# Performance work log

Hardware: AMD Instinct MI355X
Metric: run time of the kernel (lower is better)

The kernel has to match this reference:

```python
import jax, jax.numpy as jnp
import numpy as np

N_NODES = 50000
N_EDGES = 1600000
IN_CH = 32
HID = 64
K = 2


def _dconv(X, edge_index, edge_weight, W, b):
    """Diffusion graph conv (torch_geometric_temporal DConv, K=2).

    X: [N, C_in], W: [2, K, C_in, C_out], b: [C_out].
    Direction 0: forward transition P_f = D_out^{-1} A  (applied as P_f^T X).
    Direction 1: backward transition P_b = D_in^{-1} A^T (applied as P_b^T X).
    """
    n = X.shape[0]
    row, col = edge_index[0], edge_index[1]
    deg_out = jax.ops.segment_sum(edge_weight, row, num_segments=n)  # out-degree (row sums of A)
    deg_in = jax.ops.segment_sum(edge_weight, col, num_segments=n)   # in-degree  (col sums of A)
    norm_out = edge_weight / deg_out[row]  # [E]
    norm_in = edge_weight / deg_in[col]    # [E]

    # k = 0 term: identity for both directions
    H = X @ (W[0, 0] + W[1, 0])

    # k = 1 term: one diffusion step in each direction
    # forward dir: out[i] = sum_{(j->i)} w/deg_out[j] * X[j]
    Tx_o = jax.ops.segment_sum(norm_out[:, None] * X[row], col, num_segments=n)
    # backward dir: out[i] = sum_{(i->j)} w/deg_in[j] * X[j]
    Tx_i = jax.ops.segment_sum(norm_in[:, None] * X[col], row, num_segments=n)
    H = H + Tx_o @ W[0, 1] + Tx_i @ W[1, 1]
    return H + b


def setup_inputs() -> dict:
    key = jax.random.key(0)
    ks = jax.random.split(key, 12)
    cat_ch = IN_CH + HID  # GRU concatenates [X, H]
    s = 1.0 / np.sqrt(cat_ch)
    inp = {
        "x": jax.random.normal(ks[0], (N_NODES, IN_CH), dtype=jnp.float32),
        "edge_index": jax.random.randint(ks[1], (2, N_EDGES), 0, N_NODES, dtype=jnp.int32),
        "edge_weight": jax.random.uniform(ks[2], (N_EDGES,), dtype=jnp.float32, minval=0.05, maxval=1.0),
        "Wz": jax.random.uniform(ks[3], (2, K, cat_ch, HID), dtype=jnp.float32, minval=-s, maxval=s),
        "bz": jnp.zeros((HID,), dtype=jnp.float32),
        "Wr": jax.random.uniform(ks[4], (2, K, cat_ch, HID), dtype=jnp.float32, minval=-s, maxval=s),
        "br": jnp.zeros((HID,), dtype=jnp.float32),
        "Wh": jax.random.uniform(ks[5], (2, K, cat_ch, HID), dtype=jnp.float32, minval=-s, maxval=s),
        "bh": jnp.zeros((HID,), dtype=jnp.float32),
        "Wlin": jax.random.uniform(ks[6], (HID, 1), dtype=jnp.float32, minval=-1.0 / np.sqrt(HID), maxval=1.0 / np.sqrt(HID)),
        "blin": jnp.zeros((1,), dtype=jnp.float32),
    }
    return inp


def reference(x, edge_index, edge_weight, Wz, bz, Wr, br, Wh, bh, Wlin, blin):
    n = x.shape[0]
    H0 = jnp.zeros((n, HID), dtype=x.dtype)  # initial hidden state (H=None)
    XH = jnp.concatenate([x, H0], axis=-1)   # [N, IN_CH+HID]
    Z = jax.nn.sigmoid(_dconv(XH, edge_index, edge_weight, Wz, bz))
    R = jax.nn.sigmoid(_dconv(XH, edge_index, edge_weight, Wr, br))
    XHR = jnp.concatenate([x, H0 * R], axis=-1)
    H_tilde = jnp.tanh(_dconv(XHR, edge_index, edge_weight, Wh, bh))
    H = Z * H0 + (1.0 - Z) * H_tilde
    out = jnp.maximum(H, 0.0) @ Wlin + blin  # ReLU then Linear(hidden, 1)
    return out
```

## Files before the change

### kernel.cpp

```cpp
#include <hip/hip_runtime.h>
#include <math.h>

#define N_NODES 50000
#define N_EDGES 1600000
#define IN_CH 32
#define HID 64

#define NBIN 782
#define BIN_SHIFT 6
#define CHUNK 8192
#define NCHK ((N_EDGES + CHUNK - 1) / CHUNK)
#define CNTG_N (2 * NBIN * NCHK)
#define CNTG_N4 (CNTG_N / 4)
#define SCAN_BLOCKS ((CNTG_N4 + 1023) / 1024)
#define FG_CAP 2560

#define PREP_WPREP_BLOCKS 48
#define PREP_XCONV_BLOCKS ((N_NODES * 8 + 255) / 256)
#define PREP_BLOCKS (NCHK + PREP_WPREP_BLOCKS + PREP_XCONV_BLOCKS)

#define WS_RDEG_OUT 0
#define WS_RDEG_IN  50000
#define WS_CNTG     100000
#define WS_BLKSUM   406548
#define WS_WBF      406676
#define WS_BINCNT   412820
#define WS_XSB      512916
#define WS_TXO      1312916
#define WS_TXI      2112916
#define WS_XSO      2912916
#define WS_XSI      3712916
#define WS_BINNED   4512916
#define WS_END      10912916

typedef __attribute__((ext_vector_type(8))) short bf16x8;
typedef __attribute__((ext_vector_type(4))) float f32x4;

__device__ __forceinline__ unsigned short f2bf(float f) {
    unsigned int u = __float_as_uint(f);
    return (unsigned short)((u + 0x7fffu + ((u >> 16) & 1u)) >> 16);
}
__device__ __forceinline__ float bf2f(unsigned short b) {
    return __uint_as_float((unsigned int)b << 16);
}
__device__ __forceinline__ float bflo(int u) {
    return __uint_as_float(((unsigned int)u) << 16);
}
__device__ __forceinline__ float bfhi(int u) {
    return __uint_as_float(((unsigned int)u) & 0xffff0000u);
}

__global__ __launch_bounds__(256) void prep_kernel(
    const int* __restrict__ ei, const float* __restrict__ Wz,
    const float* __restrict__ Wh, const float4* __restrict__ x4,
    int* __restrict__ cntG, unsigned short* __restrict__ wbf,
    ushort4* __restrict__ xsb) {
    __shared__ int h[2 * NBIN];
    int tid = threadIdx.x;
    int b = blockIdx.x;
    if (b < NCHK) {
        for (int i = tid; i < 2 * NBIN; i += 256) h[i] = 0;
        __syncthreads();
        int e0 = b * CHUNK;
        int e1 = min(e0 + CHUNK, N_EDGES);
        for (int e = e0 + tid; e < e1; e += 256) {
            int r = ei[e];
            int c = ei[N_EDGES + e];
            atomicAdd(&h[c >> BIN_SHIFT], 1);
            atomicAdd(&h[NBIN + (r >> BIN_SHIFT)], 1);
        }
        __syncthreads();
        for (int i = tid; i < 2 * NBIN; i += 256) cntG[i * NCHK + b] = h[i];
    } else if (b < NCHK + PREP_WPREP_BLOCKS) {
        int idx = (b - NCHK) * 256 + tid;
        if (idx >= 12288) return;
        int j = idx & 7, ln = (idx >> 3) & 63, bn = (idx >> 9) & 7, kk = idx >> 12;
        int k = kk * 32 + (ln >> 4) * 8 + j;
        int n = bn * 16 + (ln & 15);
        int slab = k >> 5, c = k & 31;
        const float* W = (n < 64) ? Wz : Wh;
        int o = n & 63;
        float v;
        if (slab == 0)      v = W[c * 64 + o] + W[(2 * 96 + c) * 64 + o];
        else if (slab == 1) v = W[(96 + c) * 64 + o];
        else                v = W[(3 * 96 + c) * 64 + o];
        wbf[idx] = f2bf(v);
    } else {
        int i = (b - NCHK - PREP_WPREP_BLOCKS) * 256 + tid;
        if (i >= N_NODES * 8) return;
        float4 v = x4[i];
        ushort4 o;
        o.x = f2bf(v.x); o.y = f2bf(v.y); o.z = f2bf(v.z); o.w = f2bf(v.w);
        xsb[i] = o;
    }
}

__global__ __launch_bounds__(256) void scan_partial_kernel(
    const int4* __restrict__ cnt4, int* __restrict__ blksum, int n4) {
    __shared__ int s[256];
    int t = threadIdx.x;
    int base4 = blockIdx.x * 1024 + t * 4;
    int total = 0;
#pragma unroll
    for (int j = 0; j < 4; ++j) {
        int idx = base4 + j;
        if (idx < n4) {
            int4 v = cnt4[idx];
            total += v.x + v.y + v.z + v.w;
        }
    }
    s[t] = total;
    __syncthreads();
    for (int off = 128; off > 0; off >>= 1) {
        if (t < off) s[t] += s[t + off];
        __syncthreads();
    }
    if (t == 0) blksum[blockIdx.x] = s[0];
}

__global__ __launch_bounds__(256) void scan_blocksum_kernel(int* __restrict__ blksum, int nb) {
    __shared__ int s[256];
    int t = threadIdx.x;
    int v = (t < nb) ? blksum[t] : 0;
    s[t] = v;
    __syncthreads();
    for (int off = 1; off < 256; off <<= 1) {
        int u = (t >= off) ? s[t - off] : 0;
        __syncthreads();
        s[t] += u;
        __syncthreads();
    }
    if (t < nb) blksum[t] = s[t] - v;
}

__global__ __launch_bounds__(256) void scan_final_kernel(
    int4* __restrict__ cnt4, const int* __restrict__ blksum, int n4) {
    __shared__ int s[256];
    int t = threadIdx.x;
    int base4 = blockIdx.x * 1024 + t * 4;
    int4 vals[4];
    int total = 0;
#pragma unroll
    for (int j = 0; j < 4; ++j) {
        int idx = base4 + j;
        vals[j] = (idx < n4) ? cnt4[idx] : make_int4(0, 0, 0, 0);
        total += vals[j].x + vals[j].y + vals[j].z + vals[j].w;
    }
    s[t] = total;
    __syncthreads();
    for (int off = 1; off < 256; off <<= 1) {
        int u = (t >= off) ? s[t - off] : 0;
        __syncthreads();
        s[t] += u;
        __syncthreads();
    }
    int run = blksum[blockIdx.x] + s[t] - total;
#pragma unroll
    for (int j = 0; j < 4; ++j) {
        int idx = base4 + j;
        int4 v = vals[j];
        int4 o;
        o.x = run; run += v.x;
        o.y = run; run += v.y;
        o.z = run; run += v.z;
        o.w = run; run += v.w;
        if (idx < n4) cnt4[idx] = o;
    }
}

__global__ __launch_bounds__(512) void partition_kernel(
    const int* __restrict__ ei, const float* __restrict__ ew,
    const int* __restrict__ cntG, int2* __restrict__ binned) {
    __shared__ int2 stg[CHUNK];
    __shared__ int hist[NBIN];
    __shared__ int lst[NBIN];
    __shared__ int gStart[NBIN];
    __shared__ int sc[512];
    int tid = threadIdx.x;
    int dir = (blockIdx.x >= NCHK) ? 1 : 0;
    int chunk = blockIdx.x - dir * NCHK;

    for (int i = tid; i < NBIN; i += 512) hist[i] = 0;
    __syncthreads();

    int e0 = chunk * CHUNK;
    int n_e = min(CHUNK, N_EDGES - e0);
    int binv[16], rankv[16];
    int2 pay[16];
#pragma unroll
    for (int j = 0; j < 16; ++j) {
        int idx = tid + j * 512;
        if (idx < n_e) {
            int e = e0 + idx;
            int r = ei[e];
            int c = ei[N_EDGES + e];
            int dst = dir ? r : c;
            int src = dir ? c : r;
            int b = dst >> BIN_SHIFT;
            binv[j] = b;
            rankv[j] = atomicAdd(&hist[b], 1);
            pay[j] = make_int2((int)(((unsigned)b << 22) | ((unsigned)(dst & 63) << 16) |
                                     (unsigned)src),
                               __float_as_int(ew[e]));
        } else {
            binv[j] = -1;
        }
    }
    __syncthreads();
    int ps = (tid < 391) ? (hist[2 * tid] + hist[2 * tid + 1]) : 0;
    sc[tid] = ps;
    __syncthreads();
    for (int off = 1; off < 512; off <<= 1) {
        int u = (tid >= off) ? sc[tid - off] : 0;
        __syncthreads();
        sc[tid] += u;
        __syncthreads();
    }
    if (tid < 391) {
        int pref = sc[tid] - ps;
        lst[2 * tid] = pref;
        lst[2 * tid + 1] = pref + hist[2 * tid];
    }
    for (int i = tid; i < NBIN; i += 512)
        gStart[i] = cntG[(dir * NBIN + i) * NCHK + chunk];
    __syncthreads();
#pragma unroll
    for (int j = 0; j < 16; ++j)
        if (binv[j] >= 0) stg[lst[binv[j]] + rankv[j]] = pay[j];
    __syncthreads();
    for (int p = tid; p < n_e; p += 512) {
        int2 v2 = stg[p];
        int b = (int)(((unsigned)v2.x) >> 22);
        int gpos = gStart[b] + (p - lst[b]);
        binned[gpos] = make_int2(v2.x & 0x3FFFFF, v2.y);
    }
}

__device__ __forceinline__ void bin_range(const int* cntG, int b, int& lo, int& hi) {
    lo = cntG[b * NCHK];
    hi = (b + 1 < 2 * NBIN) ? cntG[(b + 1) * NCHK] : 2 * N_EDGES;
}

__global__ __launch_bounds__(256) void bindeg_kernel(
    const int* __restrict__ cntG, const int2* __restrict__ binned,
    const float4* __restrict__ x4, int* __restrict__ binCnt,
    ushort4* __restrict__ xso, ushort4* __restrict__ xsi) {
    __shared__ float wsum[64];
    __shared__ int cnt[64];
    int tid = threadIdx.x;
    int b = blockIdx.x;
    int dir = (b >= NBIN) ? 1 : 0;
    if (tid < 64) { wsum[tid] = 0.f; cnt[tid] = 0; }
    __syncthreads();
    int lo, hi;
    bin_range(cntG, b, lo, hi);
    for (int p = lo + tid; p < hi; p += 256) {
        int2 v = binned[p];
        int d = v.x >> 16;
        atomicAdd(&cnt[d], 1);
        atomicAdd(&wsum[d], __int_as_float(v.y));
    }
    __syncthreads();
    if (tid < 64) {
        binCnt[b * 64 + tid] = cnt[tid];
        float s = wsum[tid];
        wsum[tid] = (s != 0.f) ? (1.f / s) : 0.f;
    }
    __syncthreads();
    ushort4* xsd = dir ? xso : xsi;
    int node0 = (b - dir * NBIN) * 64;
#pragma unroll
    for (int i = tid; i < 512; i += 256) {
        int nl = i >> 3, q = i & 7;
        int node = node0 + nl;
        if (node < N_NODES) {
            float4 v = x4[node * 8 + q];
            float r = wsum[nl];
            ushort4 o;
            o.x = f2bf(v.x * r); o.y = f2bf(v.y * r);
            o.z = f2bf(v.z * r); o.w = f2bf(v.w * r);
            xsd[node * 8 + q] = o;
        }
    }
}

__global__ __launch_bounds__(256, 7) void fgather_kernel(
    const int4* __restrict__ xso4, const int4* __restrict__ xsi4,
    const int* __restrict__ cntG, const int* __restrict__ binCnt,
    const int2* __restrict__ binned, float* __restrict__ ws_f) {
    __shared__ int2 s_edge[FG_CAP];
    __shared__ int s_off[65];
    __shared__ int s_cur[64];
    __shared__ int sc[64];
    int tid = threadIdx.x;
    int b = blockIdx.x;
    int dir = (b >= NBIN) ? 1 : 0;
    int bin = b - dir * NBIN;

    int v = (tid < 64) ? binCnt[b * 64 + tid] : 0;
    if (tid < 64) sc[tid] = v;
    __syncthreads();
    for (int off = 1; off < 64; off <<= 1) {
        int u = (tid < 64 && tid >= off) ? sc[tid - off] : 0;
        __syncthreads();
        if (tid < 64) sc[tid] += u;
        __syncthreads();
    }
    if (tid < 64) {
        s_off[tid] = sc[tid] - v;
        s_cur[tid] = sc[tid] - v;
    }
    if (tid == 63) s_off[64] = sc[63];
    __syncthreads();

    int lo, hi;
    bin_range(cntG, b, lo, hi);
    int n_e = hi - lo;
    const int2* bb = binned + lo;
    for (int base = 0; base < n_e; base += 2048) {
        int2 ev[8];
#pragma unroll
        for (int j = 0; j < 8; ++j) {
            int idx = base + j * 256 + tid;
            if (idx < n_e) ev[j] = bb[idx];
        }
#pragma unroll
        for (int j = 0; j < 8; ++j) {
            int idx = base + j * 256 + tid;
            if (idx < n_e) {
                int rk = atomicAdd(&s_cur[ev[j].x >> 16], 1);
                if (rk < FG_CAP)
                    s_edge[rk] = make_int2(ev[j].x & 0xffff, ev[j].y);
            }
        }
    }
    __syncthreads();

    const int4* xsrc = dir ? xsi4 : xso4;
    int4* outp = (int4*)(ws_f + (dir == 0 ? WS_TXO : WS_TXI));
    int lane = tid & 3;
    int nl = tid >> 2;
    int p = s_off[nl], end = s_off[nl + 1];
    float acc[8];
#pragma unroll
    for (int j = 0; j < 8; ++j) acc[j] = 0.f;
    for (; p + 3 < end; p += 4) {
        int2 v0 = s_edge[p], v1 = s_edge[p + 1];
        int2 v2 = s_edge[p + 2], v3 = s_edge[p + 3];
        int4 a0 = xsrc[v0.x * 4 + lane];
        int4 a1 = xsrc[v1.x * 4 + lane];
        int4 a2 = xsrc[v2.x * 4 + lane];
        int4 a3 = xsrc[v3.x * 4 + lane];
        float c0 = __int_as_float(v0.y), c1 = __int_as_float(v1.y);
        float c2 = __int_as_float(v2.y), c3 = __int_as_float(v3.y);
        acc[0] += c0 * bflo(a0.x) + c1 * bflo(a1.x) + c2 * bflo(a2.x) + c3 * bflo(a3.x);
        acc[1] += c0 * bfhi(a0.x) + c1 * bfhi(a1.x) + c2 * bfhi(a2.x) + c3 * bfhi(a3.x);
        acc[2] += c0 * bflo(a0.y) + c1 * bflo(a1.y) + c2 * bflo(a2.y) + c3 * bflo(a3.y);
        acc[3] += c0 * bfhi(a0.y) + c1 * bfhi(a1.y) + c2 * bfhi(a2.y) + c3 * bfhi(a3.y);
        acc[4] += c0 * bflo(a0.z) + c1 * bflo(a1.z) + c2 * bflo(a2.z) + c3 * bflo(a3.z);
        acc[5] += c0 * bfhi(a0.z) + c1 * bfhi(a1.z) + c2 * bfhi(a2.z) + c3 * bfhi(a3.z);
        acc[6] += c0 * bflo(a0.w) + c1 * bflo(a1.w) + c2 * bflo(a2.w) + c3 * bflo(a3.w);
        acc[7] += c0 * bfhi(a0.w) + c1 * bfhi(a1.w) + c2 * bfhi(a2.w) + c3 * bfhi(a3.w);
    }
    for (; p < end; ++p) {
        int2 v0 = s_edge[p];
        float c0 = __int_as_float(v0.y);
        int4 a = xsrc[v0.x * 4 + lane];
        acc[0] += c0 * bflo(a.x);
        acc[1] += c0 * bfhi(a.x);
        acc[2] += c0 * bflo(a.y);
        acc[3] += c0 * bfhi(a.y);
        acc[4] += c0 * bflo(a.z);
        acc[5] += c0 * bfhi(a.z);
        acc[6] += c0 * bflo(a.w);
        acc[7] += c0 * bfhi(a.w);
    }
    int node = bin * 64 + nl;
    if (node < N_NODES) {
        int4 o;
        o.x = (int)f2bf(acc[0]) | ((int)f2bf(acc[1]) << 16);
        o.y = (int)f2bf(acc[2]) | ((int)f2bf(acc[3]) << 16);
        o.z = (int)f2bf(acc[4]) | ((int)f2bf(acc[5]) << 16);
        o.w = (int)f2bf(acc[6]) | ((int)f2bf(acc[7]) << 16);
        outp[node * 4 + lane] = o;
    }
}

#define DN_GROUP 64
#define DN_BLOCKS ((N_NODES + DN_GROUP - 1) / DN_GROUP)
__global__ __launch_bounds__(256) void dense_kernel(
    const int4* __restrict__ xsb4,
    const int4* __restrict__ txo_b, const int4* __restrict__ txi_b,
    const unsigned short* __restrict__ wbf,
    const float* __restrict__ bz, const float* __restrict__ bh,
    const float* __restrict__ Wlin, const float* __restrict__ blin,
    float* __restrict__ out) {
    __shared__ unsigned short sA[64 * 104];
    __shared__ unsigned short sB[12288];

    int tid = threadIdx.x;
    int lane = tid & 63, w = tid >> 6;
    int lm = lane & 15, quad = lane >> 4;

    for (int idx = tid; idx < 3072; idx += 256)
        *(ushort4*)&sB[idx * 4] = ((const ushort4*)wbf)[idx];

    int node0 = blockIdx.x * DN_GROUP;
    for (int idx = tid; idx < 64 * 4; idx += 256) {
        int nl = idx >> 2, q = idx & 3;
        int node = node0 + nl;
        int4 v = (node < N_NODES) ? xsb4[node * 4 + q] : make_int4(0, 0, 0, 0);
        *(int4*)&sA[nl * 104 + q * 8] = v;
    }
    for (int idx = tid; idx < 64 * 8; idx += 256) {
        int nl = idx >> 3, q = idx & 7;
        int node = node0 + nl;
        int4 v = make_int4(0, 0, 0, 0);
        if (node < N_NODES)
            v = (q < 4) ? txo_b[node * 4 + q] : txi_b[node * 4 + (q - 4)];
        *(int4*)&sA[nl * 104 + 32 + q * 8] = v;
    }

    float bzv[4], bhv[4], wlv[4];
#pragma unroll
    for (int bn = 0; bn < 4; ++bn) {
        int o = lm + 16 * bn;
        bzv[bn] = bz[o]; bhv[bn] = bh[o]; wlv[bn] = Wlin[o];
    }
    float bl = blin[0];
    __syncthreads();

    f32x4 acc[8];
#pragma unroll
    for (int bn = 0; bn < 4; ++bn) {
        acc[bn]     = (f32x4){bzv[bn], bzv[bn], bzv[bn], bzv[bn]};
        acc[bn + 4] = (f32x4){bhv[bn], bhv[bn], bhv[bn], bhv[bn]};
    }
#pragma unroll
    for (int kk = 0; kk < 3; ++kk) {
        bf16x8 af = *(const bf16x8*)&sA[(w * 16 + lm) * 104 + kk * 32 + quad * 8];
#pragma unroll
        for (int bn = 0; bn < 8; ++bn) {
            bf16x8 bf = *(const bf16x8*)&sB[((kk * 8 + bn) * 64 + lane) * 8];
            acc[bn] = __builtin_amdgcn_mfma_f32_16x16x32_bf16(af, bf, acc[bn], 0, 0, 0);
        }
    }

    float partial[4] = {0.f, 0.f, 0.f, 0.f};
#pragma unroll
    for (int bn = 0; bn < 4; ++bn) {
#pragma unroll
        for (int reg = 0; reg < 4; ++reg) {
            float az = acc[bn][reg], ah = acc[bn + 4][reg];
            float z = 1.f / (1.f + __expf(-az));
            float ht = 1.f - 2.f / (__expf(2.f * ah) + 1.f);
            partial[reg] += fmaxf((1.f - z) * ht, 0.f) * wlv[bn];
        }
    }
#pragma unroll
    for (int reg = 0; reg < 4; ++reg) {
        float s = partial[reg];
        s += __shfl_xor(s, 1, 64);
        s += __shfl_xor(s, 2, 64);
        s += __shfl_xor(s, 4, 64);
        s += __shfl_xor(s, 8, 64);
        if (lm == 0) {
            int node = node0 + w * 16 + quad * 4 + reg;
            if (node < N_NODES) out[node] = s + bl;
        }
    }
}

extern "C" void kernel_launch(void* const* d_in, const int* in_sizes, int n_in,
                              void* d_out, int out_size, void* d_ws, size_t ws_size,
                              hipStream_t stream) {
    const float* x = (const float*)d_in[0];
    const int* ei = (const int*)d_in[1];
    const float* ew = (const float*)d_in[2];
    const float* Wz = (const float*)d_in[3];
    const float* bz = (const float*)d_in[4];
    const float* Wh = (const float*)d_in[7];
    const float* bh = (const float*)d_in[8];
    const float* Wlin = (const float*)d_in[9];
    const float* blin = (const float*)d_in[10];
    float* out = (float*)d_out;
    float* wf = (float*)d_ws;
    int* wi = (int*)d_ws;
    int2* binned = (int2*)(wi + WS_BINNED);

    prep_kernel<<<PREP_BLOCKS, 256, 0, stream>>>(
        ei, Wz, Wh, (const float4*)x, wi + WS_CNTG,
        (unsigned short*)(wi + WS_WBF), (ushort4*)(wi + WS_XSB));
    scan_partial_kernel<<<SCAN_BLOCKS, 256, 0, stream>>>(
        (const int4*)(wi + WS_CNTG), wi + WS_BLKSUM, CNTG_N4);
    scan_blocksum_kernel<<<1, 256, 0, stream>>>(wi + WS_BLKSUM, SCAN_BLOCKS);
    scan_final_kernel<<<SCAN_BLOCKS, 256, 0, stream>>>(
        (int4*)(wi + WS_CNTG), wi + WS_BLKSUM, CNTG_N4);
    partition_kernel<<<2 * NCHK, 512, 0, stream>>>(ei, ew, wi + WS_CNTG, binned);
    bindeg_kernel<<<2 * NBIN, 256, 0, stream>>>(
        wi + WS_CNTG, binned, (const float4*)x, wi + WS_BINCNT,
        (ushort4*)(wi + WS_XSO), (ushort4*)(wi + WS_XSI));
    fgather_kernel<<<2 * NBIN, 256, 0, stream>>>(
        (const int4*)(wi + WS_XSO), (const int4*)(wi + WS_XSI),
        wi + WS_CNTG, wi + WS_BINCNT, binned, wf);
    dense_kernel<<<DN_BLOCKS, 256, 0, stream>>>(
        (const int4*)(wi + WS_XSB), (const int4*)(wi + WS_TXO),
        (const int4*)(wi + WS_TXI), (const unsigned short*)(wi + WS_WBF),
        bz, bh, Wlin, blin, out);
}
```

Measured before the change: 193.0 us.

## Replace histogram-scan binning with fixed-capacity bins claimed by global atomics

Drops the per-chunk edge histogram pass and the three-kernel prefix scan. Each partition block now reserves its slots in fixed-capacity per-bin buffers (FG_CAP entries) through atomicAdd on per-bin totals, and downstream kernels read bin counts straight from those totals. This removes a full pass over the edge list and several launches. In exchange, edges beyond FG_CAP in a bin are silently dropped, so correctness depends on the input's degree distribution staying under the cap, and edge order inside a bin becomes nondeterministic.

```diff
diff --git a/kernel.cpp b/kernel.cpp
--- a/kernel.cpp
+++ b/kernel.cpp
@@ -10,28 +10,22 @@
 #define BIN_SHIFT 6
 #define CHUNK 8192
 #define NCHK ((N_EDGES + CHUNK - 1) / CHUNK)
-#define CNTG_N (2 * NBIN * NCHK)
-#define CNTG_N4 (CNTG_N / 4)
-#define SCAN_BLOCKS ((CNTG_N4 + 1023) / 1024)
 #define FG_CAP 2560
 
 #define PREP_WPREP_BLOCKS 48
 #define PREP_XCONV_BLOCKS ((N_NODES * 8 + 255) / 256)
-#define PREP_BLOCKS (NCHK + PREP_WPREP_BLOCKS + PREP_XCONV_BLOCKS)
-
-#define WS_RDEG_OUT 0
-#define WS_RDEG_IN  50000
-#define WS_CNTG     100000
-#define WS_BLKSUM   406548
-#define WS_WBF      406676
-#define WS_BINCNT   412820
-#define WS_XSB      512916
-#define WS_TXO      1312916
-#define WS_TXI      2112916
-#define WS_XSO      2912916
-#define WS_XSI      3712916
-#define WS_BINNED   4512916
-#define WS_END      10912916
+#define PREP_BLOCKS (PREP_WPREP_BLOCKS + PREP_XCONV_BLOCKS + 1)
+
+#define WS_WBF      0
+#define WS_BINTOT   6144
+#define WS_BINCNT   7712
+#define WS_XSB      107808
+#define WS_TXO      907808
+#define WS_TXI      1707808
+#define WS_XSO      2507808
+#define WS_XSI      3307808
+#define WS_BINNED   4107808
+#define WS_END      12115488
 
 typedef __attribute__((ext_vector_type(8))) short bf16x8;
 typedef __attribute__((ext_vector_type(4))) float f32x4;
@@ -51,28 +45,13 @@
 }
 
 __global__ __launch_bounds__(256) void prep_kernel(
-    const int* __restrict__ ei, const float* __restrict__ Wz,
-    const float* __restrict__ Wh, const float4* __restrict__ x4,
-    int* __restrict__ cntG, unsigned short* __restrict__ wbf,
-    ushort4* __restrict__ xsb) {
-    __shared__ int h[2 * NBIN];
+    const float* __restrict__ Wz, const float* __restrict__ Wh,
+    const float4* __restrict__ x4, unsigned short* __restrict__ wbf,
+    ushort4* __restrict__ xsb, int* __restrict__ binTot) {
     int tid = threadIdx.x;
     int b = blockIdx.x;
-    if (b < NCHK) {
-        for (int i = tid; i < 2 * NBIN; i += 256) h[i] = 0;
-        __syncthreads();
-        int e0 = b * CHUNK;
-        int e1 = min(e0 + CHUNK, N_EDGES);
-        for (int e = e0 + tid; e < e1; e += 256) {
-            int r = ei[e];
-            int c = ei[N_EDGES + e];
-            atomicAdd(&h[c >> BIN_SHIFT], 1);
-            atomicAdd(&h[NBIN + (r >> BIN_SHIFT)], 1);
-        }
-        __syncthreads();
-        for (int i = tid; i < 2 * NBIN; i += 256) cntG[i * NCHK + b] = h[i];
-    } else if (b < NCHK + PREP_WPREP_BLOCKS) {
-        int idx = (b - NCHK) * 256 + tid;
+    if (b < PREP_WPREP_BLOCKS) {
+        int idx = b * 256 + tid;
         if (idx >= 12288) return;
         int j = idx & 7, ln = (idx >> 3) & 63, bn = (idx >> 9) & 7, kk = idx >> 12;
         int k = kk * 32 + (ln >> 4) * 8 + j;
@@ -85,96 +64,25 @@
         else if (slab == 1) v = W[(96 + c) * 64 + o];
         else                v = W[(3 * 96 + c) * 64 + o];
         wbf[idx] = f2bf(v);
-    } else {
-        int i = (b - NCHK - PREP_WPREP_BLOCKS) * 256 + tid;
+    } else if (b < PREP_WPREP_BLOCKS + PREP_XCONV_BLOCKS) {
+        int i = (b - PREP_WPREP_BLOCKS) * 256 + tid;
         if (i >= N_NODES * 8) return;
         float4 v = x4[i];
         ushort4 o;
         o.x = f2bf(v.x); o.y = f2bf(v.y); o.z = f2bf(v.z); o.w = f2bf(v.w);
         xsb[i] = o;
-    }
-}
-
-__global__ __launch_bounds__(256) void scan_partial_kernel(
-    const int4* __restrict__ cnt4, int* __restrict__ blksum, int n4) {
-    __shared__ int s[256];
-    int t = threadIdx.x;
-    int base4 = blockIdx.x * 1024 + t * 4;
-    int total = 0;
-#pragma unroll
-    for (int j = 0; j < 4; ++j) {
-        int idx = base4 + j;
-        if (idx < n4) {
-            int4 v = cnt4[idx];
-            total += v.x + v.y + v.z + v.w;
-        }
-    }
-    s[t] = total;
-    __syncthreads();
-    for (int off = 128; off > 0; off >>= 1) {
-        if (t < off) s[t] += s[t + off];
-        __syncthreads();
-    }
-    if (t == 0) blksum[blockIdx.x] = s[0];
-}
-
-__global__ __launch_bounds__(256) void scan_blocksum_kernel(int* __restrict__ blksum, int nb) {
-    __shared__ int s[256];
-    int t = threadIdx.x;
-    int v = (t < nb) ? blksum[t] : 0;
-    s[t] = v;
-    __syncthreads();
-    for (int off = 1; off < 256; off <<= 1) {
-        int u = (t >= off) ? s[t - off] : 0;
-        __syncthreads();
-        s[t] += u;
-        __syncthreads();
-    }
-    if (t < nb) blksum[t] = s[t] - v;
-}
-
-__global__ __launch_bounds__(256) void scan_final_kernel(
-    int4* __restrict__ cnt4, const int* __restrict__ blksum, int n4) {
-    __shared__ int s[256];
-    int t = threadIdx.x;
-    int base4 = blockIdx.x * 1024 + t * 4;
-    int4 vals[4];
-    int total = 0;
-#pragma unroll
-    for (int j = 0; j < 4; ++j) {
-        int idx = base4 + j;
-        vals[j] = (idx < n4) ? cnt4[idx] : make_int4(0, 0, 0, 0);
-        total += vals[j].x + vals[j].y + vals[j].z + vals[j].w;
-    }
-    s[t] = total;
-    __syncthreads();
-    for (int off = 1; off < 256; off <<= 1) {
-        int u = (t >= off) ? s[t - off] : 0;
-        __syncthreads();
-        s[t] += u;
-        __syncthreads();
-    }
-    int run = blksum[blockIdx.x] + s[t] - total;
-#pragma unroll
-    for (int j = 0; j < 4; ++j) {
-        int idx = base4 + j;
-        int4 v = vals[j];
-        int4 o;
-        o.x = run; run += v.x;
-        o.y = run; run += v.y;
-        o.z = run; run += v.z;
-        o.w = run; run += v.w;
-        if (idx < n4) cnt4[idx] = o;
+    } else {
+        for (int i = tid; i < 1568; i += 256) binTot[i] = 0;
     }
 }
 
 __global__ __launch_bounds__(512) void partition_kernel(
     const int* __restrict__ ei, const float* __restrict__ ew,
-    const int* __restrict__ cntG, int2* __restrict__ binned) {
+    int* __restrict__ binTot, int2* __restrict__ binned) {
     __shared__ int2 stg[CHUNK];
     __shared__ int hist[NBIN];
     __shared__ int lst[NBIN];
-    __shared__ int gStart[NBIN];
+    __shared__ int gBase[NBIN];
     __shared__ int sc[512];
     int tid = threadIdx.x;
     int dir = (blockIdx.x >= NCHK) ? 1 : 0;
@@ -222,7 +130,7 @@
         lst[2 * tid + 1] = pref + hist[2 * tid];
     }
     for (int i = tid; i < NBIN; i += 512)
-        gStart[i] = cntG[(dir * NBIN + i) * NCHK + chunk];
+        gBase[i] = (hist[i] > 0) ? atomicAdd(&binTot[dir * NBIN + i], hist[i]) : 0;
     __syncthreads();
 #pragma unroll
     for (int j = 0; j < 16; ++j)
@@ -231,18 +139,15 @@
     for (int p = tid; p < n_e; p += 512) {
         int2 v2 = stg[p];
         int b = (int)(((unsigned)v2.x) >> 22);
-        int gpos = gStart[b] + (p - lst[b]);
-        binned[gpos] = make_int2(v2.x & 0x3FFFFF, v2.y);
-    }
-}
-
-__device__ __forceinline__ void bin_range(const int* cntG, int b, int& lo, int& hi) {
-    lo = cntG[b * NCHK];
-    hi = (b + 1 < 2 * NBIN) ? cntG[(b + 1) * NCHK] : 2 * N_EDGES;
+        int off = gBase[b] + (p - lst[b]);
+        if (off < FG_CAP)
+            binned[(dir * NBIN + b) * FG_CAP + off] =
+                make_int2(v2.x & 0x3FFFFF, v2.y);
+    }
 }
 
 __global__ __launch_bounds__(256) void bindeg_kernel(
-    const int* __restrict__ cntG, const int2* __restrict__ binned,
+    const int* __restrict__ binTot, const int2* __restrict__ binned,
     const float4* __restrict__ x4, int* __restrict__ binCnt,
     ushort4* __restrict__ xso, ushort4* __restrict__ xsi) {
     __shared__ float wsum[64];
@@ -252,10 +157,10 @@
     int dir = (b >= NBIN) ? 1 : 0;
     if (tid < 64) { wsum[tid] = 0.f; cnt[tid] = 0; }
     __syncthreads();
-    int lo, hi;
-    bin_range(cntG, b, lo, hi);
-    for (int p = lo + tid; p < hi; p += 256) {
-        int2 v = binned[p];
+    int lo = b * FG_CAP;
+    int n_e = min(binTot[b], FG_CAP);
+    for (int p = tid; p < n_e; p += 256) {
+        int2 v = binned[lo + p];
         int d = v.x >> 16;
         atomicAdd(&cnt[d], 1);
         atomicAdd(&wsum[d], __int_as_float(v.y));
@@ -286,7 +191,7 @@
 
 __global__ __launch_bounds__(256, 7) void fgather_kernel(
     const int4* __restrict__ xso4, const int4* __restrict__ xsi4,
-    const int* __restrict__ cntG, const int* __restrict__ binCnt,
+    const int* __restrict__ binTot, const int* __restrict__ binCnt,
     const int2* __restrict__ binned, float* __restrict__ ws_f) {
     __shared__ int2 s_edge[FG_CAP];
     __shared__ int s_off[65];
@@ -313,10 +218,8 @@
     if (tid == 63) s_off[64] = sc[63];
     __syncthreads();
 
-    int lo, hi;
-    bin_range(cntG, b, lo, hi);
-    int n_e = hi - lo;
-    const int2* bb = binned + lo;
+    int n_e = min(binTot[b], FG_CAP);
+    const int2* bb = binned + b * FG_CAP;
     for (int base = 0; base < n_e; base += 2048) {
         int2 ev[8];
 #pragma unroll
@@ -489,20 +392,15 @@
     int2* binned = (int2*)(wi + WS_BINNED);
 
     prep_kernel<<<PREP_BLOCKS, 256, 0, stream>>>(
-        ei, Wz, Wh, (const float4*)x, wi + WS_CNTG,
-        (unsigned short*)(wi + WS_WBF), (ushort4*)(wi + WS_XSB));
-    scan_partial_kernel<<<SCAN_BLOCKS, 256, 0, stream>>>(
-        (const int4*)(wi + WS_CNTG), wi + WS_BLKSUM, CNTG_N4);
-    scan_blocksum_kernel<<<1, 256, 0, stream>>>(wi + WS_BLKSUM, SCAN_BLOCKS);
-    scan_final_kernel<<<SCAN_BLOCKS, 256, 0, stream>>>(
-        (int4*)(wi + WS_CNTG), wi + WS_BLKSUM, CNTG_N4);
-    partition_kernel<<<2 * NCHK, 512, 0, stream>>>(ei, ew, wi + WS_CNTG, binned);
+        Wz, Wh, (const float4*)x, (unsigned short*)(wi + WS_WBF),
+        (ushort4*)(wi + WS_XSB), wi + WS_BINTOT);
+    partition_kernel<<<2 * NCHK, 512, 0, stream>>>(ei, ew, wi + WS_BINTOT, binned);
     bindeg_kernel<<<2 * NBIN, 256, 0, stream>>>(
-        wi + WS_CNTG, binned, (const float4*)x, wi + WS_BINCNT,
+        wi + WS_BINTOT, binned, (const float4*)x, wi + WS_BINCNT,
         (ushort4*)(wi + WS_XSO), (ushort4*)(wi + WS_XSI));
     fgather_kernel<<<2 * NBIN, 256, 0, stream>>>(
         (const int4*)(wi + WS_XSO), (const int4*)(wi + WS_XSI),
-        wi + WS_CNTG, wi + WS_BINCNT, binned, wf);
+        wi + WS_BINTOT, wi + WS_BINCNT, binned, wf);
     dense_kernel<<<DN_BLOCKS, 256, 0, stream>>>(
         (const int4*)(wi + WS_XSB), (const int4*)(wi + WS_TXO),
         (const int4*)(wi + WS_TXI), (const unsigned short*)(wi + WS_WBF),
```

After: 168.4 us, median of 2. -12.7%, faster.
